# Performance work log

Hardware: AMD Instinct MI355X
Metric: run time of the kernel (lower is better)

## Reference

```python
import jax, jax.numpy as jnp
import numpy as np

B, HID, FH, O = 8192, 1024, 96, 8
E = O + O * (O - 1) // 2  # 36 eta params per step


def setup_inputs() -> dict:
    key = jax.random.key(0)
    ks = jax.random.split(key, 9)
    w = lambda k, sh: (jax.random.normal(k, sh, jnp.float32) * 0.02)
    return {
        "z": jax.random.normal(ks[0], (B, HID), jnp.float32),
        "W1": w(ks[1], (HID, HID)), "b1": jnp.zeros((HID,), jnp.float32),
        "W2": w(ks[2], (HID, HID)), "b2": jnp.zeros((HID,), jnp.float32),
        "Wm": w(ks[3], (HID, FH * O)), "bm": jnp.zeros((FH * O,), jnp.float32),
        "Wv": w(ks[4], (HID, FH * E)), "bv": jnp.zeros((FH * E,), jnp.float32),
    }


def reference(z, W1, b1, W2, b2, Wm, bm, Wv, bv):
    # FeedForward decoder (expansion_factor=1, dropout inactive at eval)
    h = jax.nn.silu(z @ W1 + b1) @ W2 + b2                     # [B, HID]
    means = (h @ Wm + bm).reshape(B, FH, O)                    # [B, FH, O]
    log_var = (h @ Wv + bv).reshape(B, FH, E)                  # [B, FH, E]
    eta_d = log_var[..., :O]                                   # diagonal params
    eta_T = log_var[..., O:]                                   # strict upper-tri params

    d = jnp.exp(0.5 * eta_d)                                   # [B, FH, O]
    eye = jnp.eye(O, dtype=z.dtype)
    D = d[..., :, None] * eye                                  # diag_embed(d)
    Dinv_T_scale = (1.0 / d)[..., :, None]                     # rows of D^{-1}

    iu = np.triu_indices(O, k=1)
    T = jnp.broadcast_to(eye, (B, FH, O, O)).at[..., iu[0], iu[1]].set(eta_T)

    # precision = T^T @ D^{-1} @ T ; D^{-1} @ T scales rows of T
    precision = jnp.einsum('bhji,bhjk->bhik', T, T * Dinv_T_scale)
    return means, precision, D, T
```

## Files before the change

### kernel.cpp

```cpp
#include <hip/hip_runtime.h>
#include <math.h>

#define BATCH 8192
#define HID   1024
#define FH    96
#define OO    8
#define EE    36
#define NLV   (FH*EE)
#define NM    (FH*OO)

typedef short bf16x8 __attribute__((ext_vector_type(8)));
typedef float f32x4  __attribute__((ext_vector_type(4)));

static const size_t OFF_P = (size_t)BATCH * FH * OO;
static const size_t OFF_D = OFF_P + (size_t)BATCH * FH * 64;
static const size_t OFF_T = OFF_D + (size_t)BATCH * FH * 64;

__device__ __forceinline__ unsigned short f2bf(float f) {
    unsigned int u = __float_as_uint(f);
    u += 0x7fffu + ((u >> 16) & 1u);
    return (unsigned short)(u >> 16);
}
__device__ __forceinline__ float bf2f(unsigned short s) {
    return __uint_as_float(((unsigned int)s) << 16);
}

__global__ __launch_bounds__(256) void transpose_split(const float* __restrict__ W,
                                                       unsigned short* __restrict__ Th,
                                                       unsigned short* __restrict__ Tl,
                                                       int N)
{
    __shared__ float sh[32][33];
    const int tx = threadIdx.x;
    const int ty = threadIdx.y;
    const int n0 = blockIdx.x * 32;
    const int k0 = blockIdx.y * 32;
#pragma unroll
    for (int i = 0; i < 4; ++i) {
        int kl = ty + i * 8;
        sh[kl][tx] = W[(size_t)(k0 + kl) * N + n0 + tx];
    }
    __syncthreads();
#pragma unroll
    for (int i = 0; i < 4; ++i) {
        int nl = ty + i * 8;
        float v = sh[tx][nl];
        unsigned short h = f2bf(v);
        unsigned short l = f2bf(v - bf2f(h));
        size_t o = (size_t)(n0 + nl) * HID + k0 + tx;
        Th[o] = h;
        Tl[o] = l;
    }
}

template<int ACT>
__global__ __launch_bounds__(256) void gemm_split(const float* __restrict__ A,
                                                  const unsigned short* __restrict__ Bh,
                                                  const unsigned short* __restrict__ Bl,
                                                  const float* __restrict__ bias,
                                                  float* __restrict__ C,
                                                  int N)
{
    __shared__ unsigned short AhL[128 * 32];
    __shared__ unsigned short AlL[128 * 32];
    __shared__ unsigned short BhL[128 * 32];
    __shared__ unsigned short BlL[128 * 32];

    const int tid  = threadIdx.x;
    const int lane = tid & 63;
    const int wave = tid >> 6;
    const int wm0  = (wave >> 1) * 64;
    const int wn0  = (wave & 1) * 64;
    const int m0   = blockIdx.x * 128;
    const int n0   = blockIdx.y * 128;
    const int l15  = lane & 15;
    const int l4   = lane >> 4;

    f32x4 acc[4][4];
#pragma unroll
    for (int i = 0; i < 4; ++i)
#pragma unroll
        for (int j = 0; j < 4; ++j)
            acc[i][j] = (f32x4){0.f, 0.f, 0.f, 0.f};

    for (int k0 = 0; k0 < HID; k0 += 32) {
        __syncthreads();
#pragma unroll
        for (int p = 0; p < 4; ++p) {
            int idx = p * 256 + tid;
            int ra  = idx >> 3;
            int c4  = idx & 7;
            float4 v = *reinterpret_cast<const float4*>(
                A + (size_t)(m0 + ra) * HID + k0 + c4 * 4);
            unsigned short h0 = f2bf(v.x), h1 = f2bf(v.y),
                           h2 = f2bf(v.z), h3 = f2bf(v.w);
            short4 hv = make_short4((short)h0, (short)h1, (short)h2, (short)h3);
            short4 lw = make_short4((short)f2bf(v.x - bf2f(h0)),
                                    (short)f2bf(v.y - bf2f(h1)),
                                    (short)f2bf(v.z - bf2f(h2)),
                                    (short)f2bf(v.w - bf2f(h3)));
            *reinterpret_cast<short4*>(&AhL[ra * 32 + c4 * 4]) = hv;
            *reinterpret_cast<short4*>(&AlL[ra * 32 + c4 * 4]) = lw;
        }
#pragma unroll
        for (int p = 0; p < 2; ++p) {
            int idx = p * 256 + tid;
            int rb  = idx >> 2;
            int c8  = idx & 3;
            size_t go = (size_t)(n0 + rb) * HID + k0 + c8 * 8;
            *reinterpret_cast<uint4*>(&BhL[rb * 32 + c8 * 8]) =
                *reinterpret_cast<const uint4*>(Bh + go);
            *reinterpret_cast<uint4*>(&BlL[rb * 32 + c8 * 8]) =
                *reinterpret_cast<const uint4*>(Bl + go);
        }
        __syncthreads();

        bf16x8 ah[4], al[4];
#pragma unroll
        for (int mf = 0; mf < 4; ++mf) {
            int off = (wm0 + mf * 16 + l15) * 32 + l4 * 8;
            ah[mf] = *reinterpret_cast<const bf16x8*>(&AhL[off]);
            al[mf] = *reinterpret_cast<const bf16x8*>(&AlL[off]);
        }
#pragma unroll
        for (int nf = 0; nf < 4; ++nf) {
            int off = (wn0 + nf * 16 + l15) * 32 + l4 * 8;
            bf16x8 bh = *reinterpret_cast<const bf16x8*>(&BhL[off]);
            bf16x8 bl = *reinterpret_cast<const bf16x8*>(&BlL[off]);
#pragma unroll
            for (int mf = 0; mf < 4; ++mf) {
                acc[mf][nf] = __builtin_amdgcn_mfma_f32_16x16x32_bf16(ah[mf], bh, acc[mf][nf], 0, 0, 0);
                acc[mf][nf] = __builtin_amdgcn_mfma_f32_16x16x32_bf16(ah[mf], bl, acc[mf][nf], 0, 0, 0);
                acc[mf][nf] = __builtin_amdgcn_mfma_f32_16x16x32_bf16(al[mf], bh, acc[mf][nf], 0, 0, 0);
            }
        }
    }

#pragma unroll
    for (int nf = 0; nf < 4; ++nf) {
        int gc = n0 + wn0 + nf * 16 + l15;
        float bb = bias[gc];
#pragma unroll
        for (int mf = 0; mf < 4; ++mf) {
#pragma unroll
            for (int r = 0; r < 4; ++r) {
                int gr = m0 + wm0 + mf * 16 + l4 * 4 + r;
                float o = acc[mf][nf][r] + bb;
                if (ACT) o = o / (1.f + __expf(-o));
                C[(size_t)gr * N + gc] = o;
            }
        }
    }
}

__global__ __launch_bounds__(256) void mcd_epilogue(const float* __restrict__ lv,
                                                    float* __restrict__ out)
{
    const int gid  = blockIdx.x * 256 + threadIdx.x;
    const int row  = gid / FH;
    const int head = gid - row * FH;

    const float* src = lv + (size_t)row * NLV + head * EE;
    float e[EE];
#pragma unroll
    for (int i = 0; i < 9; ++i)
        *reinterpret_cast<float4*>(&e[i * 4]) =
            reinterpret_cast<const float4*>(src)[i];

    float dv[OO], invd[OO];
#pragma unroll
    for (int i = 0; i < OO; ++i) {
        dv[i]   = __expf(0.5f * e[i]);
        invd[i] = 1.f / dv[i];
    }

    float Tu[OO][OO];
#pragma unroll
    for (int j = 0; j < OO; ++j) {
#pragma unroll
        for (int i = j + 1; i < OO; ++i) {
            Tu[j][i] = e[OO + j * 7 - (j * (j - 1)) / 2 + (i - j - 1)];
        }
    }

    float* Pp = out + OFF_P + (size_t)gid * 64;
    float* Dp = out + OFF_D + (size_t)gid * 64;
    float* Tp = out + OFF_T + (size_t)gid * 64;

#pragma unroll
    for (int i = 0; i < OO; ++i) {
        float rowv[OO];
#pragma unroll
        for (int k = 0; k < OO; ++k) {
            float s = 0.f;
#pragma unroll
            for (int j = 0; j < OO; ++j) {
                if (j <= i && j <= k) {
                    float tji = (j == i) ? 1.f : Tu[j][i];
                    float tjk = (j == k) ? 1.f : Tu[j][k];
                    s = fmaf(tji, tjk * invd[j], s);
                }
            }
            rowv[k] = s;
        }
        *reinterpret_cast<float4*>(Pp + i * 8)     = make_float4(rowv[0], rowv[1], rowv[2], rowv[3]);
        *reinterpret_cast<float4*>(Pp + i * 8 + 4) = make_float4(rowv[4], rowv[5], rowv[6], rowv[7]);
    }

#pragma unroll
    for (int i = 0; i < OO; ++i) {
        float rowv[OO];
#pragma unroll
        for (int k = 0; k < OO; ++k) rowv[k] = (k == i) ? dv[i] : 0.f;
        *reinterpret_cast<float4*>(Dp + i * 8)     = make_float4(rowv[0], rowv[1], rowv[2], rowv[3]);
        *reinterpret_cast<float4*>(Dp + i * 8 + 4) = make_float4(rowv[4], rowv[5], rowv[6], rowv[7]);
    }

#pragma unroll
    for (int j = 0; j < OO; ++j) {
        float rowv[OO];
#pragma unroll
        for (int k = 0; k < OO; ++k)
            rowv[k] = (k < j) ? 0.f : (k == j) ? 1.f : Tu[j][k];
        *reinterpret_cast<float4*>(Tp + j * 8)     = make_float4(rowv[0], rowv[1], rowv[2], rowv[3]);
        *reinterpret_cast<float4*>(Tp + j * 8 + 4) = make_float4(rowv[4], rowv[5], rowv[6], rowv[7]);
    }
}

extern "C" void kernel_launch(void* const* d_in, const int* in_sizes, int n_in,
                              void* d_out, int out_size, void* d_ws, size_t ws_size,
                              hipStream_t stream)
{
    (void)in_sizes; (void)n_in; (void)out_size; (void)ws_size;
    const float* z  = (const float*)d_in[0];
    const float* W1 = (const float*)d_in[1];
    const float* b1 = (const float*)d_in[2];
    const float* W2 = (const float*)d_in[3];
    const float* b2 = (const float*)d_in[4];
    const float* Wm = (const float*)d_in[5];
    const float* bm = (const float*)d_in[6];
    const float* Wv = (const float*)d_in[7];
    const float* bv = (const float*)d_in[8];
    float* out = (float*)d_out;

    float* h1 = (float*)d_ws;
    float* h  = h1 + (size_t)BATCH * HID;
    float* lv = h  + (size_t)BATCH * HID;
    unsigned short* us = (unsigned short*)(lv + (size_t)BATCH * NLV);
    unsigned short* W1h = us;                 us += (size_t)HID * HID;
    unsigned short* W1l = us;                 us += (size_t)HID * HID;
    unsigned short* W2h = us;                 us += (size_t)HID * HID;
    unsigned short* W2l = us;                 us += (size_t)HID * HID;
    unsigned short* Wmh = us;                 us += (size_t)NM * HID;
    unsigned short* Wml = us;                 us += (size_t)NM * HID;
    unsigned short* Wvh = us;                 us += (size_t)NLV * HID;
    unsigned short* Wvl = us;

    dim3 tb(32, 8);
    transpose_split<<<dim3(HID / 32, HID / 32), tb, 0, stream>>>(W1, W1h, W1l, HID);
    transpose_split<<<dim3(HID / 32, HID / 32), tb, 0, stream>>>(W2, W2h, W2l, HID);
    transpose_split<<<dim3(NM  / 32, HID / 32), tb, 0, stream>>>(Wm, Wmh, Wml, NM);
    transpose_split<<<dim3(NLV / 32, HID / 32), tb, 0, stream>>>(Wv, Wvh, Wvl, NLV);

    gemm_split<1><<<dim3(BATCH / 128, HID / 128), 256, 0, stream>>>(z,  W1h, W1l, b1, h1, HID);
    gemm_split<0><<<dim3(BATCH / 128, HID / 128), 256, 0, stream>>>(h1, W2h, W2l, b2, h,  HID);
    gemm_split<0><<<dim3(BATCH / 128, NM  / 128), 256, 0, stream>>>(h,  Wmh, Wml, bm, out, NM);
    gemm_split<0><<<dim3(BATCH / 128, NLV / 128), 256, 0, stream>>>(h,  Wvh, Wvl, bv, lv, NLV);

    mcd_epilogue<<<dim3(BATCH * FH / 256), 256, 0, stream>>>(lv, out);
}
```

Before: 1.276 ms.

## Pre-split activations into blocked bf16 hi/lo layout and load via global_load_lds

Activations are now converted to bf16 hi/lo pairs once, either in a separate blockify kernel for z or in the GEMM epilogue for the hidden layers. They are stored in a k-group-major blocked layout that matches the MFMA fragment order, and the weights are transposed into the same layout. The GEMM inner loop then stages tiles with direct global-to-LDS 16-byte loads instead of per-tile float loads and repeated splitting. This removes redundant conversion work across N-blocks and halves activation traffic. The cost is an extra conversion pass, scattered 2-byte stores in the epilogue, and workspace aliasing between zh/zl/h1 and lv.

```diff
diff --git a/kernel.cpp b/kernel.cpp
--- a/kernel.cpp
+++ b/kernel.cpp
@@ -9,8 +9,9 @@
 #define NLV   (FH*EE)
 #define NM    (FH*OO)
 
-typedef short bf16x8 __attribute__((ext_vector_type(8)));
-typedef float f32x4  __attribute__((ext_vector_type(4)));
+typedef short  bf16x8 __attribute__((ext_vector_type(8)));
+typedef float  f32x4  __attribute__((ext_vector_type(4)));
+typedef unsigned short u16x8 __attribute__((ext_vector_type(8)));
 
 static const size_t OFF_P = (size_t)BATCH * FH * OO;
 static const size_t OFF_D = OFF_P + (size_t)BATCH * FH * 64;
@@ -25,10 +26,44 @@
     return __uint_as_float(((unsigned int)s) << 16);
 }
 
-__global__ __launch_bounds__(256) void transpose_split(const float* __restrict__ W,
-                                                       unsigned short* __restrict__ Th,
-                                                       unsigned short* __restrict__ Tl,
-                                                       int N)
+__device__ __forceinline__ size_t blk_off(int r, int k) {
+    return ((size_t)(r >> 7)) * (128 * HID) + (size_t)(k >> 3) * 1024
+         + (size_t)(r & 127) * 8 + (size_t)(k & 7);
+}
+
+__device__ __forceinline__ void glds16(const unsigned short* g, unsigned short* l) {
+    __builtin_amdgcn_global_load_lds(
+        (const __attribute__((address_space(1))) unsigned int*)g,
+        (__attribute__((address_space(3))) unsigned int*)l, 16, 0, 0);
+}
+
+__global__ __launch_bounds__(256) void conv_blockify(const float* __restrict__ X,
+                                                     unsigned short* __restrict__ Xh,
+                                                     unsigned short* __restrict__ Xl)
+{
+    int idx  = blockIdx.x * 256 + threadIdx.x;
+    int row  = idx & 127;
+    int kgrp = (idx >> 7) & 127;
+    int rblk = idx >> 14;
+    const float* src = X + ((size_t)(rblk * 128 + row)) * HID + kgrp * 8;
+    float4 v0 = reinterpret_cast<const float4*>(src)[0];
+    float4 v1 = reinterpret_cast<const float4*>(src)[1];
+    float vv[8] = {v0.x, v0.y, v0.z, v0.w, v1.x, v1.y, v1.z, v1.w};
+    u16x8 h, l;
+#pragma unroll
+    for (int j = 0; j < 8; ++j) {
+        unsigned short hh = f2bf(vv[j]);
+        h[j] = hh;
+        l[j] = f2bf(vv[j] - bf2f(hh));
+    }
+    *reinterpret_cast<u16x8*>(Xh + (size_t)idx * 8) = h;
+    *reinterpret_cast<u16x8*>(Xl + (size_t)idx * 8) = l;
+}
+
+__global__ __launch_bounds__(256) void transpose_split_blk(const float* __restrict__ W,
+                                                           unsigned short* __restrict__ Th,
+                                                           unsigned short* __restrict__ Tl,
+                                                           int N)
 {
     __shared__ float sh[32][33];
     const int tx = threadIdx.x;
@@ -47,35 +82,41 @@
         float v = sh[tx][nl];
         unsigned short h = f2bf(v);
         unsigned short l = f2bf(v - bf2f(h));
-        size_t o = (size_t)(n0 + nl) * HID + k0 + tx;
+        size_t o = blk_off(n0 + nl, k0 + tx);
         Th[o] = h;
         Tl[o] = l;
     }
 }
 
-template<int ACT>
-__global__ __launch_bounds__(256) void gemm_split(const float* __restrict__ A,
-                                                  const unsigned short* __restrict__ Bh,
-                                                  const unsigned short* __restrict__ Bl,
-                                                  const float* __restrict__ bias,
-                                                  float* __restrict__ C,
-                                                  int N)
-{
-    __shared__ unsigned short AhL[128 * 32];
-    __shared__ unsigned short AlL[128 * 32];
-    __shared__ unsigned short BhL[128 * 32];
-    __shared__ unsigned short BlL[128 * 32];
+template<int ACT, int OUTBLK>
+__global__ __launch_bounds__(256) void gemm_bs(
+    const unsigned short* __restrict__ Ah_, const unsigned short* __restrict__ Al_,
+    const unsigned short* __restrict__ Bh_, const unsigned short* __restrict__ Bl_,
+    const float* __restrict__ bias,
+    float* __restrict__ Cf,
+    unsigned short* __restrict__ Ch, unsigned short* __restrict__ Cl,
+    int N)
+{
+    __shared__ unsigned short AhL[4096];
+    __shared__ unsigned short AlL[4096];
+    __shared__ unsigned short BhL[4096];
+    __shared__ unsigned short BlL[4096];
 
     const int tid  = threadIdx.x;
     const int lane = tid & 63;
     const int wave = tid >> 6;
+    const int m0   = blockIdx.x * 128;
+    const int n0   = blockIdx.y * 128;
     const int wm0  = (wave >> 1) * 64;
     const int wn0  = (wave & 1) * 64;
-    const int m0   = blockIdx.x * 128;
-    const int n0   = blockIdx.y * 128;
     const int l15  = lane & 15;
     const int l4   = lane >> 4;
 
+    const unsigned short* Ah = Ah_ + (size_t)(m0 >> 7) * (128 * HID);
+    const unsigned short* Al = Al_ + (size_t)(m0 >> 7) * (128 * HID);
+    const unsigned short* Bh = Bh_ + (size_t)(n0 >> 7) * (128 * HID);
+    const unsigned short* Bl = Bl_ + (size_t)(n0 >> 7) * (128 * HID);
+
     f32x4 acc[4][4];
 #pragma unroll
     for (int i = 0; i < 4; ++i)
@@ -83,55 +124,41 @@
         for (int j = 0; j < 4; ++j)
             acc[i][j] = (f32x4){0.f, 0.f, 0.f, 0.f};
 
+    const int c0 = wave * 2;
+    const int c1 = c0 + 1;
+
     for (int k0 = 0; k0 < HID; k0 += 32) {
         __syncthreads();
-#pragma unroll
-        for (int p = 0; p < 4; ++p) {
-            int idx = p * 256 + tid;
-            int ra  = idx >> 3;
-            int c4  = idx & 7;
-            float4 v = *reinterpret_cast<const float4*>(
-                A + (size_t)(m0 + ra) * HID + k0 + c4 * 4);
-            unsigned short h0 = f2bf(v.x), h1 = f2bf(v.y),
-                           h2 = f2bf(v.z), h3 = f2bf(v.w);
-            short4 hv = make_short4((short)h0, (short)h1, (short)h2, (short)h3);
-            short4 lw = make_short4((short)f2bf(v.x - bf2f(h0)),
-                                    (short)f2bf(v.y - bf2f(h1)),
-                                    (short)f2bf(v.z - bf2f(h2)),
-                                    (short)f2bf(v.w - bf2f(h3)));
-            *reinterpret_cast<short4*>(&AhL[ra * 32 + c4 * 4]) = hv;
-            *reinterpret_cast<short4*>(&AlL[ra * 32 + c4 * 4]) = lw;
-        }
-#pragma unroll
-        for (int p = 0; p < 2; ++p) {
-            int idx = p * 256 + tid;
-            int rb  = idx >> 2;
-            int c8  = idx & 3;
-            size_t go = (size_t)(n0 + rb) * HID + k0 + c8 * 8;
-            *reinterpret_cast<uint4*>(&BhL[rb * 32 + c8 * 8]) =
-                *reinterpret_cast<const uint4*>(Bh + go);
-            *reinterpret_cast<uint4*>(&BlL[rb * 32 + c8 * 8]) =
-                *reinterpret_cast<const uint4*>(Bl + go);
-        }
+        const size_t tb = (size_t)(k0 >> 3) * 1024;
+        const size_t o0 = tb + (size_t)c0 * 512 + (size_t)lane * 8;
+        const size_t o1 = tb + (size_t)c1 * 512 + (size_t)lane * 8;
+        glds16(Ah + o0, AhL + c0 * 512);
+        glds16(Ah + o1, AhL + c1 * 512);
+        glds16(Al + o0, AlL + c0 * 512);
+        glds16(Al + o1, AlL + c1 * 512);
+        glds16(Bh + o0, BhL + c0 * 512);
+        glds16(Bh + o1, BhL + c1 * 512);
+        glds16(Bl + o0, BlL + c0 * 512);
+        glds16(Bl + o1, BlL + c1 * 512);
         __syncthreads();
 
-        bf16x8 ah[4], al[4];
+        bf16x8 a_h[4], a_l[4];
 #pragma unroll
         for (int mf = 0; mf < 4; ++mf) {
-            int off = (wm0 + mf * 16 + l15) * 32 + l4 * 8;
-            ah[mf] = *reinterpret_cast<const bf16x8*>(&AhL[off]);
-            al[mf] = *reinterpret_cast<const bf16x8*>(&AlL[off]);
+            int off = l4 * 1024 + (wm0 + mf * 16 + l15) * 8;
+            a_h[mf] = *reinterpret_cast<const bf16x8*>(&AhL[off]);
+            a_l[mf] = *reinterpret_cast<const bf16x8*>(&AlL[off]);
         }
 #pragma unroll
         for (int nf = 0; nf < 4; ++nf) {
-            int off = (wn0 + nf * 16 + l15) * 32 + l4 * 8;
-            bf16x8 bh = *reinterpret_cast<const bf16x8*>(&BhL[off]);
-            bf16x8 bl = *reinterpret_cast<const bf16x8*>(&BlL[off]);
+            int off = l4 * 1024 + (wn0 + nf * 16 + l15) * 8;
+            bf16x8 b_h = *reinterpret_cast<const bf16x8*>(&BhL[off]);
+            bf16x8 b_l = *reinterpret_cast<const bf16x8*>(&BlL[off]);
 #pragma unroll
             for (int mf = 0; mf < 4; ++mf) {
-                acc[mf][nf] = __builtin_amdgcn_mfma_f32_16x16x32_bf16(ah[mf], bh, acc[mf][nf], 0, 0, 0);
-                acc[mf][nf] = __builtin_amdgcn_mfma_f32_16x16x32_bf16(ah[mf], bl, acc[mf][nf], 0, 0, 0);
-                acc[mf][nf] = __builtin_amdgcn_mfma_f32_16x16x32_bf16(al[mf], bh, acc[mf][nf], 0, 0, 0);
+                acc[mf][nf] = __builtin_amdgcn_mfma_f32_16x16x32_bf16(a_h[mf], b_h, acc[mf][nf], 0, 0, 0);
+                acc[mf][nf] = __builtin_amdgcn_mfma_f32_16x16x32_bf16(a_h[mf], b_l, acc[mf][nf], 0, 0, 0);
+                acc[mf][nf] = __builtin_amdgcn_mfma_f32_16x16x32_bf16(a_l[mf], b_h, acc[mf][nf], 0, 0, 0);
             }
         }
     }
@@ -147,7 +174,15 @@
                 int gr = m0 + wm0 + mf * 16 + l4 * 4 + r;
                 float o = acc[mf][nf][r] + bb;
                 if (ACT) o = o / (1.f + __expf(-o));
-                C[(size_t)gr * N + gc] = o;
+                if (OUTBLK == 0) {
+                    Cf[(size_t)gr * N + gc] = o;
+                } else {
+                    unsigned short h = f2bf(o);
+                    unsigned short l = f2bf(o - bf2f(h));
+                    size_t off = blk_off(gr, gc);
+                    Ch[off] = h;
+                    Cl[off] = l;
+                }
             }
         }
     }
@@ -243,29 +278,39 @@
     const float* bv = (const float*)d_in[8];
     float* out = (float*)d_out;
 
-    float* h1 = (float*)d_ws;
-    float* h  = h1 + (size_t)BATCH * HID;
-    float* lv = h  + (size_t)BATCH * HID;
-    unsigned short* us = (unsigned short*)(lv + (size_t)BATCH * NLV);
-    unsigned short* W1h = us;                 us += (size_t)HID * HID;
-    unsigned short* W1l = us;                 us += (size_t)HID * HID;
-    unsigned short* W2h = us;                 us += (size_t)HID * HID;
-    unsigned short* W2l = us;                 us += (size_t)HID * HID;
-    unsigned short* Wmh = us;                 us += (size_t)NM * HID;
-    unsigned short* Wml = us;                 us += (size_t)NM * HID;
-    unsigned short* Wvh = us;                 us += (size_t)NLV * HID;
-    unsigned short* Wvl = us;
+    const size_t EL = (size_t)BATCH * HID;
+
+    float* lv = (float*)d_ws;
+    unsigned short* zh  = (unsigned short*)d_ws;
+    unsigned short* zl  = zh  + EL;
+    unsigned short* h1h = zl  + EL;
+    unsigned short* h1l = h1h + EL;
+    unsigned short* hh  = (unsigned short*)(lv + (size_t)BATCH * NLV);
+    unsigned short* hl  = hh  + EL;
+    unsigned short* W1h = hl  + EL;
+    unsigned short* W1l = W1h + (size_t)HID * HID;
+    unsigned short* W2h = W1l + (size_t)HID * HID;
+    unsigned short* W2l = W2h + (size_t)HID * HID;
+    unsigned short* Wmh = W2l + (size_t)HID * HID;
+    unsigned short* Wml = Wmh + (size_t)NM * HID;
+    unsigned short* Wvh = Wml + (size_t)NM * HID;
+    unsigned short* Wvl = Wvh + (size_t)NLV * HID;
 
     dim3 tb(32, 8);
-    transpose_split<<<dim3(HID / 32, HID / 32), tb, 0, stream>>>(W1, W1h, W1l, HID);
-    transpose_split<<<dim3(HID / 32, HID / 32), tb, 0, stream>>>(W2, W2h, W2l, HID);
-    transpose_split<<<dim3(NM  / 32, HID / 32), tb, 0, stream>>>(Wm, Wmh, Wml, NM);
-    transpose_split<<<dim3(NLV / 32, HID / 32), tb, 0, stream>>>(Wv, Wvh, Wvl, NLV);
-
-    gemm_split<1><<<dim3(BATCH / 128, HID / 128), 256, 0, stream>>>(z,  W1h, W1l, b1, h1, HID);
-    gemm_split<0><<<dim3(BATCH / 128, HID / 128), 256, 0, stream>>>(h1, W2h, W2l, b2, h,  HID);
-    gemm_split<0><<<dim3(BATCH / 128, NM  / 128), 256, 0, stream>>>(h,  Wmh, Wml, bm, out, NM);
-    gemm_split<0><<<dim3(BATCH / 128, NLV / 128), 256, 0, stream>>>(h,  Wvh, Wvl, bv, lv, NLV);
+    conv_blockify<<<dim3(4096), 256, 0, stream>>>(z, zh, zl);
+    transpose_split_blk<<<dim3(HID / 32, HID / 32), tb, 0, stream>>>(W1, W1h, W1l, HID);
+    transpose_split_blk<<<dim3(HID / 32, HID / 32), tb, 0, stream>>>(W2, W2h, W2l, HID);
+    transpose_split_blk<<<dim3(NM  / 32, HID / 32), tb, 0, stream>>>(Wm, Wmh, Wml, NM);
+    transpose_split_blk<<<dim3(NLV / 32, HID / 32), tb, 0, stream>>>(Wv, Wvh, Wvl, NLV);
+
+    gemm_bs<1, 1><<<dim3(BATCH / 128, HID / 128), 256, 0, stream>>>(
+        zh, zl, W1h, W1l, b1, nullptr, h1h, h1l, HID);
+    gemm_bs<0, 1><<<dim3(BATCH / 128, HID / 128), 256, 0, stream>>>(
+        h1h, h1l, W2h, W2l, b2, nullptr, hh, hl, HID);
+    gemm_bs<0, 0><<<dim3(BATCH / 128, NM / 128), 256, 0, stream>>>(
+        hh, hl, Wmh, Wml, bm, out, nullptr, nullptr, NM);
+    gemm_bs<0, 0><<<dim3(BATCH / 128, NLV / 128), 256, 0, stream>>>(
+        hh, hl, Wvh, Wvl, bv, lv, nullptr, nullptr, NLV);
 
     mcd_epilogue<<<dim3(BATCH * FH / 256), 256, 0, stream>>>(lv, out);
 }
```

New measurement: 1.184 ms. 7.2% less time.
